# Optimization experiments

Measured on AMD Instinct MI355X. Metric: run time of the kernel, lower is better.

Reference implementation:

```python
import jax, jax.numpy as jnp
import numpy as np

N = 50000   # nodes
E = 500000  # edges
D = 128     # enc_dim == Hout
INIT_W = 0.1


def _lin_w(k, din, dout):
    return jax.random.normal(k, (dout, din), jnp.float32) * INIT_W


def setup_inputs() -> dict:
    key = jax.random.key(0)
    ks = jax.random.split(key, 16)
    inp = {
        "x": jax.random.normal(ks[0], (N, D), jnp.float32),
        "src": jax.random.randint(ks[1], (E,), 0, N),
        "dst": jax.random.randint(ks[2], (E,), 0, N),
        # encoders (Linear enc_dim -> enc_dim)
        "WencK": _lin_w(ks[3], D, D), "bencK": jnp.zeros((D,), jnp.float32),
        "WencP1": _lin_w(ks[4], D, D), "bencP1": jnp.zeros((D,), jnp.float32),
        "WencP2": _lin_w(ks[5], D, D), "bencP2": jnp.zeros((D,), jnp.float32),
        # Kfun: Linear-Tanh-Linear-ReLU-Linear
        "K0W": _lin_w(ks[6], D, D), "K0b": jnp.zeros((D,), jnp.float32),
        "K1W": _lin_w(ks[7], D, D), "K1b": jnp.zeros((D,), jnp.float32),
        "K2W": _lin_w(ks[8], D, D), "K2b": jnp.zeros((D,), jnp.float32),
        # Ufun: Linear-Tanh-Linear-ReLU-Linear
        "U0W": _lin_w(ks[9], D, D), "U0b": jnp.zeros((D,), jnp.float32),
        "U1W": _lin_w(ks[10], D, D), "U1b": jnp.zeros((D,), jnp.float32),
        "U2W": _lin_w(ks[11], D, D), "U2b": jnp.zeros((D,), jnp.float32),
    }
    return inp


def _mlp3(h, W0, b0, W1, b1, W2, b2):
    h = jnp.tanh(h @ W0.T + b0)
    h = jax.nn.relu(h @ W1.T + b1)
    return h @ W2.T + b2


def reference(x, src, dst,
              WencK, bencK, WencP1, bencP1, WencP2, bencP2,
              K0W, K0b, K1W, K1b, K2W, K2b,
              U0W, U0b, U1W, U1b, U2W, U2b):
    # getK: encode nodes, copy_u + sum to dst, node MLP
    h1 = x @ WencK.T + bencK                                   # [N, D]
    h1_agg = jax.ops.segment_sum(h1[src], dst, num_segments=N)  # [N, D]
    Knode = _mlp3(h1_agg, K0W, K0b, K1W, K1b, K2W, K2b)         # [N, D]
    # getU: u_add_v on encoded features, edge MLP
    p1 = x @ WencP1.T + bencP1
    p2 = x @ WencP2.T + bencP2
    Eedge = _mlp3(p1[src] + p2[dst], U0W, U0b, U1W, U1b, U2W, U2b)  # [E, D]
    # getH: u_mul_e + sum to dst
    Enew = jax.ops.segment_sum(Knode[src] * Eedge, dst, num_segments=N)  # [N, D]
    return jnp.sum(Enew)
```

## Files before the change

### kernel.cpp

```cpp
#include <hip/hip_runtime.h>
#include <math.h>

#define NN 50000
#define NE 500000
#define DD 128
#define STR 136
#define NSCAN (2 * NN)
#define NBLK ((NSCAN + 1023) / 1024)

typedef __attribute__((ext_vector_type(8))) short short8;
typedef __attribute__((ext_vector_type(4))) float floatx4;

__device__ __forceinline__ float bf2f(unsigned short u) {
    unsigned v = ((unsigned)u) << 16;
    float f;
    __builtin_memcpy(&f, &v, 4);
    return f;
}
__device__ __forceinline__ unsigned short f2bf(float f) {
    unsigned x;
    __builtin_memcpy(&x, &f, 4);
    x += 0x7FFF + ((x >> 16) & 1);
    return (unsigned short)(x >> 16);
}
__device__ __forceinline__ float fast_tanh(float x) {
    float t = __builtin_amdgcn_exp2f(x * 2.88539008177793f);
    return 1.f - 2.f * __builtin_amdgcn_rcpf(t + 1.f);
}

__global__ __launch_bounds__(256) void composite_kernel(
    const float* __restrict__ U0W, const float* __restrict__ WencP1,
    const float* __restrict__ WencP2, const float* __restrict__ K0W,
    const float* __restrict__ WencK,
    const float* __restrict__ bp1, const float* __restrict__ bp2,
    const float* __restrict__ U0b, const float* __restrict__ bk,
    const float* __restrict__ U2b,
    float* __restrict__ comp, float* __restrict__ bvecs)
{
    int b = blockIdx.x;
    int t = threadIdx.x;
    if (b == 6) {
        if (t < 128) {
            float s1 = 0.f, s2 = 0.f;
            for (int k = 0; k < DD; ++k) {
                s1 += U0W[t * DD + k] * (bp1[k] + bp2[k]);
                s2 += K0W[t * DD + k] * bk[k];
            }
            bvecs[t] = s1 + U0b[t];
            bvecs[128 + t] = s2;
            int f = (t & 64) + 16 * (t & 3) + ((t & 63) >> 2);
            bvecs[256 + t] = U2b[f];
        }
        return;
    }
    __shared__ float Bs[DD * DD];
    int mat = b >> 1, half = b & 1;
    const float* A = (mat == 2) ? K0W : U0W;
    const float* B = (mat == 0) ? WencP1 : (mat == 1) ? WencP2 : WencK;
    float* C = comp + (size_t)mat * DD * DD;
    for (int i = 0; i < 64; ++i)
        Bs[i * 256 + t] = B[i * 256 + t];
    __syncthreads();
    int row = half * 64 + (t >> 2);
    int j0 = (t & 3) * 32;
    float acc[32];
    #pragma unroll
    for (int jj = 0; jj < 32; ++jj) acc[jj] = 0.f;
    for (int k = 0; k < DD; ++k) {
        float a = A[row * DD + k];
        #pragma unroll
        for (int jj = 0; jj < 32; ++jj)
            acc[jj] += a * Bs[k * DD + j0 + jj];
    }
    #pragma unroll
    for (int jj = 0; jj < 32; ++jj) C[row * DD + j0 + jj] = acc[jj];
}

__global__ __launch_bounds__(256) void preconv_kernel(
    const float* __restrict__ comp, const float* __restrict__ K1W,
    const float* __restrict__ K2W, const float* __restrict__ U2W,
    const float* __restrict__ U1W, unsigned short* __restrict__ out)
{
    int g = blockIdx.x * 256 + threadIdx.x;
    if (g >= 7 * 2048) return;
    int m = g >> 11;
    int rem = g & 2047;
    int kt = rem >> 9, nt = (rem >> 6) & 7, lane = rem & 63;
    const float* W;
    bool perm = false, tr = false;
    switch (m) {
        case 0: W = comp; break;
        case 1: W = comp + 16384; break;
        case 2: W = comp + 32768; break;
        case 3: W = K1W; perm = true; break;
        case 4: W = K2W; perm = true; break;
        case 5: W = U2W; perm = true; tr = true; break;
        default: W = U1W; break;
    }
    int n = nt * 16 + (lane & 15);
    #pragma unroll
    for (int j = 0; j < 8; ++j) {
        int ks = kt * 32 + (lane >> 4) * 8 + j;
        int f = perm ? (ks & 64) + 16 * (ks & 3) + ((ks & 63) >> 2) : ks;
        float v = tr ? W[f * DD + n] : W[n * DD + f];
        out[(size_t)g * 8 + j] = f2bf(v);
    }
}

__global__ __launch_bounds__(256) void hist_kernel(
    const int* __restrict__ src, const int* __restrict__ dst,
    int* __restrict__ cnt_dst, int* __restrict__ cnt_src,
    int* __restrict__ rank_d, int* __restrict__ rank_s)
{
    int e = blockIdx.x * 256 + threadIdx.x;
    if (e < NE) {
        rank_d[e] = atomicAdd(&cnt_dst[dst[e]], 1);
        rank_s[e] = atomicAdd(&cnt_src[src[e]], 1);
    }
}

__global__ __launch_bounds__(1024) void scan1_kernel(
    const int* __restrict__ cnt, int* __restrict__ base, int* __restrict__ bsum)
{
    __shared__ int wsum[16];
    int t = threadIdx.x;
    int i = blockIdx.x * 1024 + t;
    int v = (i < NSCAN) ? cnt[i] : 0;
    int lane = t & 63, w = t >> 6;
    int x = v;
    #pragma unroll
    for (int off = 1; off < 64; off <<= 1) {
        int y = __shfl_up(x, off);
        if (lane >= off) x += y;
    }
    if (lane == 63) wsum[w] = x;
    __syncthreads();
    if (w == 0) {
        int s = (lane < 16) ? wsum[lane] : 0;
        #pragma unroll
        for (int off = 1; off < 16; off <<= 1) {
            int y = __shfl_up(s, off);
            if (lane >= off) s += y;
        }
        if (lane < 16) wsum[lane] = s;
    }
    __syncthreads();
    int wavebase = (w == 0) ? 0 : wsum[w - 1];
    int incl = wavebase + x;
    if (i < NSCAN) base[i] = incl - v;
    if (t == 1023) bsum[blockIdx.x] = incl;
}

__global__ __launch_bounds__(128) void scan2_kernel(
    int* __restrict__ bsum, float* __restrict__ out)
{
    if (threadIdx.x == 0 && blockIdx.x == 0) *out = 0.f;
    __shared__ int wsum[2];
    int t = threadIdx.x;
    int v = (t < NBLK) ? bsum[t] : 0;
    int lane = t & 63, w = t >> 6;
    int x = v;
    #pragma unroll
    for (int off = 1; off < 64; off <<= 1) {
        int y = __shfl_up(x, off);
        if (lane >= off) x += y;
    }
    if (lane == 63) wsum[w] = x;
    __syncthreads();
    int wavebase = (w == 0) ? 0 : wsum[0];
    int incl = wavebase + x;
    if (t < NBLK) bsum[t] = incl - v;
}

__global__ __launch_bounds__(1024) void scan3_kernel(
    int* __restrict__ base, const int* __restrict__ bsum)
{
    int i = blockIdx.x * 1024 + threadIdx.x;
    if (i < NSCAN) base[i] += bsum[blockIdx.x];
}

__global__ __launch_bounds__(256) void place_kernel(
    const int* __restrict__ src, const int* __restrict__ dst,
    const int* __restrict__ base,
    const int* __restrict__ rank_d, const int* __restrict__ rank_s,
    int* __restrict__ sorted_src_bydst,
    int* __restrict__ sorted_dst_bysrc, int* __restrict__ sorted_sid_bysrc)
{
    int e = blockIdx.x * 256 + threadIdx.x;
    if (e < NE) {
        int s = src[e], d = dst[e];
        sorted_src_bydst[base[d] + rank_d[e]] = s;
        int p = base[NN + s] + rank_s[e] - NE;
        sorted_dst_bysrc[p] = d;
        sorted_sid_bysrc[p] = s;
    }
}

__global__ __launch_bounds__(256) void enc_kernel(
    const float* __restrict__ x, const unsigned short* __restrict__ wf,
    const float* __restrict__ bvecs,
    unsigned short* __restrict__ q1, unsigned short* __restrict__ q2,
    unsigned short* __restrict__ xbf)
{
    __shared__ unsigned short A[128 * STR];
    const int t = threadIdx.x;
    const int lane = t & 63, w = t >> 6;
    const int wm = w >> 1, wn = w & 1;
    const int c = lane & 15, q = lane >> 4;
    const int row0 = blockIdx.x * 128;

    #pragma unroll
    for (int i = 0; i < 16; ++i) {
        int idx = i * 256 + t;
        int r = idx >> 5, ch = idx & 31;
        int gr = row0 + r;
        ushort4 v4 = {0, 0, 0, 0};
        if (gr < NN) {
            float4 f = *(const float4*)&x[(size_t)gr * DD + ch * 4];
            v4.x = f2bf(f.x); v4.y = f2bf(f.y); v4.z = f2bf(f.z); v4.w = f2bf(f.w);
            *(ushort4*)&xbf[(size_t)gr * DD + ch * 4] = v4;
        }
        *(ushort4*)&A[r * STR + ch * 4] = v4;
    }
    __syncthreads();

    for (int l = 0; l < 2; ++l) {
        floatx4 acc[4][4];
        #pragma unroll
        for (int i = 0; i < 4; ++i)
            #pragma unroll
            for (int j = 0; j < 4; ++j)
                acc[i][j] = (floatx4){0.f, 0.f, 0.f, 0.f};
        const short8* W8 = (const short8*)(wf + (size_t)l * 16384);
        #pragma unroll
        for (int kt = 0; kt < 4; ++kt) {
            short8 af[4], bfr[4];
            #pragma unroll
            for (int i = 0; i < 4; ++i)
                af[i] = *(const short8*)&A[(wm * 64 + i * 16 + c) * STR + kt * 32 + q * 8];
            #pragma unroll
            for (int j = 0; j < 4; ++j)
                bfr[j] = W8[(kt * 8 + wn * 4 + j) * 64 + lane];
            #pragma unroll
            for (int i = 0; i < 4; ++i)
                #pragma unroll
                for (int j = 0; j < 4; ++j)
                    acc[i][j] = __builtin_amdgcn_mfma_f32_16x16x32_bf16(af[i], bfr[j], acc[i][j], 0, 0, 0);
        }
        unsigned short* pp = (l == 0) ? q1 : q2;
        float bv[4];
        #pragma unroll
        for (int j = 0; j < 4; ++j)
            bv[j] = (l == 0) ? bvecs[c + 16 * j + 64 * wn] : 0.f;

        #pragma unroll
        for (int i = 0; i < 4; ++i)
            #pragma unroll
            for (int r = 0; r < 4; ++r) {
                int node = row0 + wm * 64 + i * 16 + 4 * q + r;
                if (node < NN) {
                    #pragma unroll
                    for (int j = 0; j < 4; ++j)
                        pp[(size_t)node * DD + c + 16 * j + 64 * wn] = f2bf(acc[i][j][r] + bv[j]);
                }
            }
    }
}

__global__ __launch_bounds__(256) void agg_kernel(
    const unsigned short* __restrict__ xbf,
    const int* __restrict__ base, const int* __restrict__ cnt,
    const int* __restrict__ sorted_src,
    unsigned short* __restrict__ xagg)
{
    int wave = blockIdx.x * 4 + (threadIdx.x >> 6);
    int lane = threadIdx.x & 63;
    if (wave >= NN) return;
    int lo = base[wave];
    int hi = lo + cnt[wave];
    float ax = 0.f, ay = 0.f;
    for (int off = lo; off < hi; off += 64) {
        int myid = (off + lane < hi) ? sorted_src[off + lane] : 0;
        int nk = min(64, hi - off);
        int k = 0;
        for (; k + 4 <= nk; k += 4) {
            int s0 = __shfl(myid, k);
            int s1 = __shfl(myid, k + 1);
            int s2 = __shfl(myid, k + 2);
            int s3 = __shfl(myid, k + 3);
            ushort2 v0 = *(const ushort2*)&xbf[(size_t)s0 * DD + lane * 2];
            ushort2 v1 = *(const ushort2*)&xbf[(size_t)s1 * DD + lane * 2];
            ushort2 v2 = *(const ushort2*)&xbf[(size_t)s2 * DD + lane * 2];
            ushort2 v3 = *(const ushort2*)&xbf[(size_t)s3 * DD + lane * 2];
            ax += bf2f(v0.x) + bf2f(v1.x) + bf2f(v2.x) + bf2f(v3.x);
            ay += bf2f(v0.y) + bf2f(v1.y) + bf2f(v2.y) + bf2f(v3.y);
        }
        for (; k < nk; ++k) {
            int s = __shfl(myid, k);
            ushort2 v = *(const ushort2*)&xbf[(size_t)s * DD + lane * 2];
            ax += bf2f(v.x);
            ay += bf2f(v.y);
        }
    }
    ushort2 o;
    o.x = f2bf(ax); o.y = f2bf(ay);
    *(ushort2*)&xagg[(size_t)wave * DD + lane * 2] = o;
}

__global__ __launch_bounds__(256) void node_kernel(
    const unsigned short* __restrict__ xagg, const unsigned short* __restrict__ wf,
    const int* __restrict__ cnt, const float* __restrict__ bvecs,
    const float* __restrict__ K0b, const float* __restrict__ K1b,
    const float* __restrict__ K2b,
    unsigned short* __restrict__ Km, float* __restrict__ kb)
{
    __shared__ unsigned short A[128 * STR];
    const int t = threadIdx.x;
    const int lane = t & 63, w = t >> 6;
    const int wm = w >> 1, wn = w & 1;
    const int c = lane & 15, q = lane >> 4;
    const int row0 = blockIdx.x * 128;

    #pragma unroll
    for (int i = 0; i < 8; ++i) {
        int idx = i * 256 + t;
        int r = idx >> 4, ch = idx & 15;
        int gr = row0 + r;
        short8 v = (short8){0,0,0,0,0,0,0,0};
        if (gr < NN) v = *(const short8*)&xagg[(size_t)gr * DD + ch * 8];
        *(short8*)&A[r * STR + ch * 8] = v;
    }
    __syncthreads();

    for (int l = 0; l < 4; ++l) {
        floatx4 acc[4][4];
        #pragma unroll
        for (int i = 0; i < 4; ++i)
            #pragma unroll
            for (int j = 0; j < 4; ++j)
                acc[i][j] = (floatx4){0.f, 0.f, 0.f, 0.f};
        const short8* W8 = (const short8*)(wf + (size_t)(2 + l) * 16384);
        #pragma unroll
        for (int kt = 0; kt < 4; ++kt) {
            short8 af[4], bfr[4];
            #pragma unroll
            for (int i = 0; i < 4; ++i)
                af[i] = *(const short8*)&A[(wm * 64 + i * 16 + c) * STR + kt * 32 + q * 8];
            #pragma unroll
            for (int j = 0; j < 4; ++j)
                bfr[j] = W8[(kt * 8 + wn * 4 + j) * 64 + lane];
            #pragma unroll
            for (int i = 0; i < 4; ++i)
                #pragma unroll
                for (int j = 0; j < 4; ++j)
                    acc[i][j] = __builtin_amdgcn_mfma_f32_16x16x32_bf16(af[i], bfr[j], acc[i][j], 0, 0, 0);
        }

        if (l < 3) {
            const float* bb = (l == 0) ? K0b : (l == 1) ? K1b : K2b;
            float bv[4];
            #pragma unroll
            for (int j = 0; j < 4; ++j) bv[j] = bb[c + 16 * j + 64 * wn];
            float bvv[4];
            #pragma unroll
            for (int j = 0; j < 4; ++j)
                bvv[j] = (l == 0) ? bvecs[128 + c + 16 * j + 64 * wn] : 0.f;

            __syncthreads();
            #pragma unroll
            for (int i = 0; i < 4; ++i)
                #pragma unroll
                for (int r = 0; r < 4; ++r) {
                    int node = row0 + wm * 64 + i * 16 + 4 * q + r;
                    float cn = (l == 0) ? (float)((node < NN) ? cnt[node] : 0) : 0.f;
                    float v0 = acc[i][0][r] + bv[0] + cn * bvv[0];
                    float v1 = acc[i][1][r] + bv[1] + cn * bvv[1];
                    float v2 = acc[i][2][r] + bv[2] + cn * bvv[2];
                    float v3 = acc[i][3][r] + bv[3] + cn * bvv[3];
                    if (l == 0) {
                        v0 = fast_tanh(v0); v1 = fast_tanh(v1);
                        v2 = fast_tanh(v2); v3 = fast_tanh(v3);
                    } else if (l == 1) {
                        v0 = fmaxf(v0, 0.f); v1 = fmaxf(v1, 0.f);
                        v2 = fmaxf(v2, 0.f); v3 = fmaxf(v3, 0.f);
                    }
                    ushort4 pk;
                    pk.x = f2bf(v0); pk.y = f2bf(v1); pk.z = f2bf(v2); pk.w = f2bf(v3);
                    int m = wm * 64 + i * 16 + 4 * q + r;
                    *(ushort4*)&A[m * STR + 4 * c + 64 * wn] = pk;
                }
            __syncthreads();

            if (l == 2) {
                if (t < 128) {
                    int node = row0 + t;
                    if (node < NN) {
                        float s = 0.f;
                        #pragma unroll
                        for (int ch = 0; ch < 16; ++ch) {
                            short8 v = *(const short8*)&A[t * STR + ch * 8];
                            #pragma unroll
                            for (int e = 0; e < 8; ++e)
                                s += bf2f((unsigned short)v[e]) * bvecs[256 + ch * 8 + e];
                        }
                        kb[node] = s;
                    }
                }
            }
        } else {
            #pragma unroll
            for (int i = 0; i < 4; ++i)
                #pragma unroll
                for (int r = 0; r < 4; ++r) {
                    int node = row0 + wm * 64 + i * 16 + 4 * q + r;
                    if (node < NN) {
                        ushort4 pk;
                        pk.x = f2bf(acc[i][0][r]);
                        pk.y = f2bf(acc[i][1][r]);
                        pk.z = f2bf(acc[i][2][r]);
                        pk.w = f2bf(acc[i][3][r]);
                        *(ushort4*)&Km[(size_t)node * DD + 4 * c + 64 * wn] = pk;
                    }
                }
        }
    }
}

__global__ __launch_bounds__(256) void edge_kernel(
    const unsigned short* __restrict__ q1, const unsigned short* __restrict__ q2,
    const unsigned short* __restrict__ Km, const float* __restrict__ kb,
    const int* __restrict__ sorted_sid, const int* __restrict__ sorted_dst,
    const unsigned short* __restrict__ wf, const float* __restrict__ U1b,
    float* __restrict__ out)
{
    __shared__ unsigned short A[128 * STR];
    __shared__ int sidx[128];
    __shared__ int didx[128];
    __shared__ float red[4];
    const int t = threadIdx.x;
    const int lane = t & 63, w = t >> 6;
    const int wm = w >> 1, wn = w & 1;
    const int c = lane & 15, q = lane >> 4;
    const int e0 = blockIdx.x * 128;

    if (t < 128) {
        int e = e0 + t;
        sidx[t] = (e < NE) ? sorted_sid[e] : -1;
        didx[t] = (e < NE) ? sorted_dst[e] : 0;
    }
    __syncthreads();

    float part = 0.f;
    if (t < 128 && sidx[t] >= 0) part += kb[sidx[t]];

    #pragma unroll
    for (int i = 0; i < 8; ++i) {
        int idx = i * 256 + t;
        int r = idx >> 4, ch = idx & 15;
        int s = sidx[r];
        short8 o8 = (short8){0,0,0,0,0,0,0,0};
        if (s >= 0) {
            short8 a8 = *(const short8*)&q1[(size_t)s * DD + ch * 8];
            short8 b8 = *(const short8*)&q2[(size_t)didx[r] * DD + ch * 8];
            #pragma unroll
            for (int k = 0; k < 8; ++k)
                o8[k] = (short)f2bf(fast_tanh(bf2f((unsigned short)a8[k]) + bf2f((unsigned short)b8[k])));
        }
        *(short8*)&A[r * STR + ch * 8] = o8;
    }
    __syncthreads();

    floatx4 acc[4][4];
    #pragma unroll
    for (int i = 0; i < 4; ++i)
        #pragma unroll
        for (int j = 0; j < 4; ++j)
            acc[i][j] = (floatx4){0.f, 0.f, 0.f, 0.f};
    const short8* W8 = (const short8*)(wf + (size_t)6 * 16384);
    #pragma unroll
    for (int kt = 0; kt < 4; ++kt) {
        short8 af[4], bfr[4];
        #pragma unroll
        for (int i = 0; i < 4; ++i)
            af[i] = *(const short8*)&A[(wm * 64 + i * 16 + c) * STR + kt * 32 + q * 8];
        #pragma unroll
        for (int j = 0; j < 4; ++j)
            bfr[j] = W8[(kt * 8 + wn * 4 + j) * 64 + lane];
        #pragma unroll
        for (int i = 0; i < 4; ++i)
            #pragma unroll
            for (int j = 0; j < 4; ++j)
                acc[i][j] = __builtin_amdgcn_mfma_f32_16x16x32_bf16(af[i], bfr[j], acc[i][j], 0, 0, 0);
    }
    float bv[4];
    #pragma unroll
    for (int j = 0; j < 4; ++j) bv[j] = U1b[c + 16 * j + 64 * wn];

    #pragma unroll
    for (int i = 0; i < 4; ++i)
        #pragma unroll
        for (int r = 0; r < 4; ++r) {
            int m = wm * 64 + i * 16 + 4 * q + r;
            int s = sidx[m];
            if (s >= 0) {
                ushort4 km4 = *(const ushort4*)&Km[(size_t)s * DD + 4 * c + 64 * wn];
                part += fmaxf(acc[i][0][r] + bv[0], 0.f) * bf2f(km4.x)
                      + fmaxf(acc[i][1][r] + bv[1], 0.f) * bf2f(km4.y)
                      + fmaxf(acc[i][2][r] + bv[2], 0.f) * bf2f(km4.z)
                      + fmaxf(acc[i][3][r] + bv[3], 0.f) * bf2f(km4.w);
            }
        }

    #pragma unroll
    for (int off = 32; off > 0; off >>= 1)
        part += __shfl_down(part, off);
    if (lane == 0) red[w] = part;
    __syncthreads();
    if (t == 0)
        atomicAdd(out, red[0] + red[1] + red[2] + red[3]);
}

extern "C" void kernel_launch(void* const* d_in, const int* in_sizes, int n_in,
                              void* d_out, int out_size, void* d_ws, size_t ws_size,
                              hipStream_t stream)
{
    const float* x     = (const float*)d_in[0];
    const int*   src   = (const int*)  d_in[1];
    const int*   dst   = (const int*)  d_in[2];
    const float* WencK = (const float*)d_in[3];
    const float* bencK = (const float*)d_in[4];
    const float* WencP1= (const float*)d_in[5];
    const float* bencP1= (const float*)d_in[6];
    const float* WencP2= (const float*)d_in[7];
    const float* bencP2= (const float*)d_in[8];
    const float* K0W   = (const float*)d_in[9];
    const float* K0b   = (const float*)d_in[10];
    const float* K1W   = (const float*)d_in[11];
    const float* K1b   = (const float*)d_in[12];
    const float* K2W   = (const float*)d_in[13];
    const float* K2b   = (const float*)d_in[14];
    const float* U0W   = (const float*)d_in[15];
    const float* U0b   = (const float*)d_in[16];
    const float* U1W   = (const float*)d_in[17];
    const float* U1b   = (const float*)d_in[18];
    const float* U2W   = (const float*)d_in[19];
    const float* U2b   = (const float*)d_in[20];

    char* ws = (char*)d_ws;
    unsigned short* wfrag = (unsigned short*)ws;
    float* comp  = (float*)(ws + 0x40000);
    float* bvecs = (float*)(ws + 0x70000);
    unsigned short* xbf  = (unsigned short*)(ws + 0x71000);
    unsigned short* q1   = xbf + (size_t)NN * DD;
    unsigned short* q2   = q1 + (size_t)NN * DD;
    unsigned short* Kmg  = q2 + (size_t)NN * DD;
    unsigned short* xagg = Kmg + (size_t)NN * DD;
    float* kb       = (float*)(xagg + (size_t)NN * DD);
    int* cnt_dst    = (int*)(kb + NN);
    int* cnt_src    = cnt_dst + NN;
    int* base       = cnt_src + NN;
    int* bsum       = base + NSCAN;
    int* rank_d     = bsum + 128;
    int* rank_s     = rank_d + NE;
    int* sorted_src_bydst = rank_s + NE;
    int* sorted_dst_bysrc = sorted_src_bydst + NE;
    int* sorted_sid_bysrc = sorted_dst_bysrc + NE;

    hipMemsetAsync(cnt_dst, 0, 2 * NN * sizeof(int), stream);

    composite_kernel<<<7, 256, 0, stream>>>(
        U0W, WencP1, WencP2, K0W, WencK, bencP1, bencP2, U0b, bencK, U2b,
        comp, bvecs);

    preconv_kernel<<<(7 * 2048 + 255) / 256, 256, 0, stream>>>(
        comp, K1W, K2W, U2W, U1W, wfrag);

    hist_kernel<<<(NE + 255) / 256, 256, 0, stream>>>(
        src, dst, cnt_dst, cnt_src, rank_d, rank_s);

    scan1_kernel<<<NBLK, 1024, 0, stream>>>(cnt_dst, base, bsum);
    scan2_kernel<<<1, 128, 0, stream>>>(bsum, (float*)d_out);
    scan3_kernel<<<NBLK, 1024, 0, stream>>>(base, bsum);

    place_kernel<<<(NE + 255) / 256, 256, 0, stream>>>(
        src, dst, base, rank_d, rank_s,
        sorted_src_bydst, sorted_dst_bysrc, sorted_sid_bysrc);

    enc_kernel<<<(NN + 127) / 128, 256, 0, stream>>>(
        x, wfrag, bvecs, q1, q2, xbf);

    agg_kernel<<<(NN + 3) / 4, 256, 0, stream>>>(
        xbf, base, cnt_dst, sorted_src_bydst, xagg);

    node_kernel<<<(NN + 127) / 128, 256, 0, stream>>>(
        xagg, wfrag, cnt_dst, bvecs, K0b, K1b, K2b, Kmg, kb);

    edge_kernel<<<(NE + 127) / 128, 256, 0, stream>>>(
        q1, q2, Kmg, kb, sorted_sid_bysrc, sorted_dst_bysrc, wfrag, U1b,
        (float*)d_out);
}
```

Before: 342.2 us.

## Merge independent setup kernels into fewer launches and pack edge index pairs

Merges several small, independent kernels into shared launches that pick their role by block index. Histogram, x-to-bf16 conversion and weight composition share one launch. Preconversion shares a launch with the first scan pass, and the encoder GEMM shares one with the node MLP. Edge (src,dst) pairs are stored as a single int2 array, and each edge block now processes two 128-edge tiles, which halves the number of atomics on the output. The goal is to cut launch count and serial gaps. The cost is less parallelism per launch and a larger shared-memory footprint in merged blocks, since the 64KB Bs array is now declared in histogram blocks too, which may reduce occupancy.

```diff
diff --git a/kernel.cpp b/kernel.cpp
--- a/kernel.cpp
+++ b/kernel.cpp
@@ -1,4 +1,5 @@
 #include <hip/hip_runtime.h>
+#include <hip/hip_bf16.h>
 #include <math.h>
 
 #define NN 50000
@@ -6,7 +7,11 @@
 #define DD 128
 #define STR 136
 #define NSCAN (2 * NN)
-#define NBLK ((NSCAN + 1023) / 1024)
+#define SCAN_BLK ((NSCAN + 1023) / 1024)
+#define HIST_BLK ((NE + 255) / 256)
+#define CVT_BLK  ((NN * DD + 4095) / 4096)
+#define PRECONV_BLK ((7 * 2048 + 1023) / 1024)
+#define ENC_BLK  ((NN + 127) / 128)
 
 typedef __attribute__((ext_vector_type(8))) short short8;
 typedef __attribute__((ext_vector_type(4))) float floatx4;
@@ -28,7 +33,11 @@
     return 1.f - 2.f * __builtin_amdgcn_rcpf(t + 1.f);
 }
 
-__global__ __launch_bounds__(256) void composite_kernel(
+__global__ __launch_bounds__(256) void k1_kernel(
+    const int* __restrict__ src, const int* __restrict__ dst,
+    int* __restrict__ cnt_dst, int* __restrict__ cnt_src,
+    int* __restrict__ rank_d, int* __restrict__ rank_s,
+    const float* __restrict__ x, unsigned short* __restrict__ xbf,
     const float* __restrict__ U0W, const float* __restrict__ WencP1,
     const float* __restrict__ WencP2, const float* __restrict__ K0W,
     const float* __restrict__ WencK,
@@ -37,8 +46,35 @@
     const float* __restrict__ U2b,
     float* __restrict__ comp, float* __restrict__ bvecs)
 {
-    int b = blockIdx.x;
+    __shared__ float Bs[DD * DD];
+    int blk = blockIdx.x;
     int t = threadIdx.x;
+
+    if (blk < HIST_BLK) {
+        int e = blk * 256 + t;
+        if (e < NE) {
+            rank_d[e] = atomicAdd(&cnt_dst[dst[e]], 1);
+            rank_s[e] = atomicAdd(&cnt_src[src[e]], 1);
+        }
+        return;
+    }
+    if (blk < HIST_BLK + CVT_BLK) {
+        int base = (blk - HIST_BLK) * 4096;
+        #pragma unroll
+        for (int j = 0; j < 4; ++j) {
+            int idx = base + (j * 256 + t) * 4;
+            if (idx < NN * DD) {
+                float4 f = *(const float4*)&x[idx];
+                ushort4 v4;
+                v4.x = f2bf(f.x); v4.y = f2bf(f.y);
+                v4.z = f2bf(f.z); v4.w = f2bf(f.w);
+                *(ushort4*)&xbf[idx] = v4;
+            }
+        }
+        return;
+    }
+
+    int b = blk - (HIST_BLK + CVT_BLK);
     if (b == 6) {
         if (t < 128) {
             float s1 = 0.f, s2 = 0.f;
@@ -53,7 +89,6 @@
         }
         return;
     }
-    __shared__ float Bs[DD * DD];
     int mat = b >> 1, half = b & 1;
     const float* A = (mat == 2) ? K0W : U0W;
     const float* B = (mat == 0) ? WencP1 : (mat == 1) ? WencP2 : WencK;
@@ -76,56 +111,76 @@
     for (int jj = 0; jj < 32; ++jj) C[row * DD + j0 + jj] = acc[jj];
 }
 
-__global__ __launch_bounds__(256) void preconv_kernel(
+__global__ __launch_bounds__(1024) void k2_kernel(
     const float* __restrict__ comp, const float* __restrict__ K1W,
     const float* __restrict__ K2W, const float* __restrict__ U2W,
-    const float* __restrict__ U1W, unsigned short* __restrict__ out)
-{
-    int g = blockIdx.x * 256 + threadIdx.x;
-    if (g >= 7 * 2048) return;
-    int m = g >> 11;
-    int rem = g & 2047;
-    int kt = rem >> 9, nt = (rem >> 6) & 7, lane = rem & 63;
-    const float* W;
-    bool perm = false, tr = false;
-    switch (m) {
-        case 0: W = comp; break;
-        case 1: W = comp + 16384; break;
-        case 2: W = comp + 32768; break;
-        case 3: W = K1W; perm = true; break;
-        case 4: W = K2W; perm = true; break;
-        case 5: W = U2W; perm = true; tr = true; break;
-        default: W = U1W; break;
-    }
-    int n = nt * 16 + (lane & 15);
+    const float* __restrict__ U1W, unsigned short* __restrict__ wfrag,
+    const int* __restrict__ cnt, int* __restrict__ base, int* __restrict__ bsum)
+{
+    int t = threadIdx.x;
+    if (blockIdx.x < PRECONV_BLK) {
+        int g = blockIdx.x * 1024 + t;
+        if (g >= 7 * 2048) return;
+        int m = g >> 11;
+        int rem = g & 2047;
+        int kt = rem >> 9, nt = (rem >> 6) & 7, lane = rem & 63;
+        const float* W;
+        bool perm = false, tr = false;
+        switch (m) {
+            case 0: W = comp; break;
+            case 1: W = comp + 16384; break;
+            case 2: W = comp + 32768; break;
+            case 3: W = K1W; perm = true; break;
+            case 4: W = K2W; perm = true; break;
+            case 5: W = U2W; perm = true; tr = true; break;
+            default: W = U1W; break;
+        }
+        int n = nt * 16 + (lane & 15);
+        #pragma unroll
+        for (int j = 0; j < 8; ++j) {
+            int ks = kt * 32 + (lane >> 4) * 8 + j;
+            int f = perm ? (ks & 64) + 16 * (ks & 3) + ((ks & 63) >> 2) : ks;
+            float v = tr ? W[f * DD + n] : W[n * DD + f];
+            wfrag[(size_t)g * 8 + j] = f2bf(v);
+        }
+        return;
+    }
+    __shared__ int wsum[16];
+    int sb = blockIdx.x - PRECONV_BLK;
+    int i = sb * 1024 + t;
+    int v = (i < NSCAN) ? cnt[i] : 0;
+    int lane = t & 63, w = t >> 6;
+    int xv = v;
     #pragma unroll
-    for (int j = 0; j < 8; ++j) {
-        int ks = kt * 32 + (lane >> 4) * 8 + j;
-        int f = perm ? (ks & 64) + 16 * (ks & 3) + ((ks & 63) >> 2) : ks;
-        float v = tr ? W[f * DD + n] : W[n * DD + f];
-        out[(size_t)g * 8 + j] = f2bf(v);
-    }
-}
-
-__global__ __launch_bounds__(256) void hist_kernel(
-    const int* __restrict__ src, const int* __restrict__ dst,
-    int* __restrict__ cnt_dst, int* __restrict__ cnt_src,
-    int* __restrict__ rank_d, int* __restrict__ rank_s)
-{
-    int e = blockIdx.x * 256 + threadIdx.x;
-    if (e < NE) {
-        rank_d[e] = atomicAdd(&cnt_dst[dst[e]], 1);
-        rank_s[e] = atomicAdd(&cnt_src[src[e]], 1);
-    }
-}
-
-__global__ __launch_bounds__(1024) void scan1_kernel(
-    const int* __restrict__ cnt, int* __restrict__ base, int* __restrict__ bsum)
-{
-    __shared__ int wsum[16];
+    for (int off = 1; off < 64; off <<= 1) {
+        int y = __shfl_up(xv, off);
+        if (lane >= off) xv += y;
+    }
+    if (lane == 63) wsum[w] = xv;
+    __syncthreads();
+    if (w == 0) {
+        int s = (lane < 16) ? wsum[lane] : 0;
+        #pragma unroll
+        for (int off = 1; off < 16; off <<= 1) {
+            int y = __shfl_up(s, off);
+            if (lane >= off) s += y;
+        }
+        if (lane < 16) wsum[lane] = s;
+    }
+    __syncthreads();
+    int wavebase = (w == 0) ? 0 : wsum[w - 1];
+    int incl = wavebase + xv;
+    if (i < NSCAN) base[i] = incl - v;
+    if (t == 1023) bsum[sb] = incl;
+}
+
+__global__ __launch_bounds__(128) void scan2_kernel(
+    int* __restrict__ bsum, float* __restrict__ out)
+{
+    if (threadIdx.x == 0 && blockIdx.x == 0) *out = 0.f;
+    __shared__ int wsum[2];
     int t = threadIdx.x;
-    int i = blockIdx.x * 1024 + t;
-    int v = (i < NSCAN) ? cnt[i] : 0;
+    int v = (t < SCAN_BLK) ? bsum[t] : 0;
     int lane = t & 63, w = t >> 6;
     int x = v;
     #pragma unroll
@@ -135,41 +190,9 @@
     }
     if (lane == 63) wsum[w] = x;
     __syncthreads();
-    if (w == 0) {
-        int s = (lane < 16) ? wsum[lane] : 0;
-        #pragma unroll
-        for (int off = 1; off < 16; off <<= 1) {
-            int y = __shfl_up(s, off);
-            if (lane >= off) s += y;
-        }
-        if (lane < 16) wsum[lane] = s;
-    }
-    __syncthreads();
-    int wavebase = (w == 0) ? 0 : wsum[w - 1];
-    int incl = wavebase + x;
-    if (i < NSCAN) base[i] = incl - v;
-    if (t == 1023) bsum[blockIdx.x] = incl;
-}
-
-__global__ __launch_bounds__(128) void scan2_kernel(
-    int* __restrict__ bsum, float* __restrict__ out)
-{
-    if (threadIdx.x == 0 && blockIdx.x == 0) *out = 0.f;
-    __shared__ int wsum[2];
-    int t = threadIdx.x;
-    int v = (t < NBLK) ? bsum[t] : 0;
-    int lane = t & 63, w = t >> 6;
-    int x = v;
-    #pragma unroll
-    for (int off = 1; off < 64; off <<= 1) {
-        int y = __shfl_up(x, off);
-        if (lane >= off) x += y;
-    }
-    if (lane == 63) wsum[w] = x;
-    __syncthreads();
     int wavebase = (w == 0) ? 0 : wsum[0];
     int incl = wavebase + x;
-    if (t < NBLK) bsum[t] = incl - v;
+    if (t < SCAN_BLK) bsum[t] = incl - v;
 }
 
 __global__ __launch_bounds__(1024) void scan3_kernel(
@@ -183,87 +206,14 @@
     const int* __restrict__ src, const int* __restrict__ dst,
     const int* __restrict__ base,
     const int* __restrict__ rank_d, const int* __restrict__ rank_s,
-    int* __restrict__ sorted_src_bydst,
-    int* __restrict__ sorted_dst_bysrc, int* __restrict__ sorted_sid_bysrc)
+    int* __restrict__ sorted_src_bydst, int2* __restrict__ epairs)
 {
     int e = blockIdx.x * 256 + threadIdx.x;
     if (e < NE) {
         int s = src[e], d = dst[e];
         sorted_src_bydst[base[d] + rank_d[e]] = s;
         int p = base[NN + s] + rank_s[e] - NE;
-        sorted_dst_bysrc[p] = d;
-        sorted_sid_bysrc[p] = s;
-    }
-}
-
-__global__ __launch_bounds__(256) void enc_kernel(
-    const float* __restrict__ x, const unsigned short* __restrict__ wf,
-    const float* __restrict__ bvecs,
-    unsigned short* __restrict__ q1, unsigned short* __restrict__ q2,
-    unsigned short* __restrict__ xbf)
-{
-    __shared__ unsigned short A[128 * STR];
-    const int t = threadIdx.x;
-    const int lane = t & 63, w = t >> 6;
-    const int wm = w >> 1, wn = w & 1;
-    const int c = lane & 15, q = lane >> 4;
-    const int row0 = blockIdx.x * 128;
-
-    #pragma unroll
-    for (int i = 0; i < 16; ++i) {
-        int idx = i * 256 + t;
-        int r = idx >> 5, ch = idx & 31;
-        int gr = row0 + r;
-        ushort4 v4 = {0, 0, 0, 0};
-        if (gr < NN) {
-            float4 f = *(const float4*)&x[(size_t)gr * DD + ch * 4];
-            v4.x = f2bf(f.x); v4.y = f2bf(f.y); v4.z = f2bf(f.z); v4.w = f2bf(f.w);
-            *(ushort4*)&xbf[(size_t)gr * DD + ch * 4] = v4;
-        }
-        *(ushort4*)&A[r * STR + ch * 4] = v4;
-    }
-    __syncthreads();
-
-    for (int l = 0; l < 2; ++l) {
-        floatx4 acc[4][4];
-        #pragma unroll
-        for (int i = 0; i < 4; ++i)
-            #pragma unroll
-            for (int j = 0; j < 4; ++j)
-                acc[i][j] = (floatx4){0.f, 0.f, 0.f, 0.f};
-        const short8* W8 = (const short8*)(wf + (size_t)l * 16384);
-        #pragma unroll
-        for (int kt = 0; kt < 4; ++kt) {
-            short8 af[4], bfr[4];
-            #pragma unroll
-            for (int i = 0; i < 4; ++i)
-                af[i] = *(const short8*)&A[(wm * 64 + i * 16 + c) * STR + kt * 32 + q * 8];
-            #pragma unroll
-            for (int j = 0; j < 4; ++j)
-                bfr[j] = W8[(kt * 8 + wn * 4 + j) * 64 + lane];
-            #pragma unroll
-            for (int i = 0; i < 4; ++i)
-                #pragma unroll
-                for (int j = 0; j < 4; ++j)
-                    acc[i][j] = __builtin_amdgcn_mfma_f32_16x16x32_bf16(af[i], bfr[j], acc[i][j], 0, 0, 0);
-        }
-        unsigned short* pp = (l == 0) ? q1 : q2;
-        float bv[4];
-        #pragma unroll
-        for (int j = 0; j < 4; ++j)
-            bv[j] = (l == 0) ? bvecs[c + 16 * j + 64 * wn] : 0.f;
-
-        #pragma unroll
-        for (int i = 0; i < 4; ++i)
-            #pragma unroll
-            for (int r = 0; r < 4; ++r) {
-                int node = row0 + wm * 64 + i * 16 + 4 * q + r;
-                if (node < NN) {
-                    #pragma unroll
-                    for (int j = 0; j < 4; ++j)
-                        pp[(size_t)node * DD + c + 16 * j + 64 * wn] = f2bf(acc[i][j][r] + bv[j]);
-                }
-            }
+        epairs[p] = make_int2(s, d);
     }
 }
 
@@ -307,11 +257,13 @@
     *(ushort2*)&xagg[(size_t)wave * DD + lane * 2] = o;
 }
 
-__global__ __launch_bounds__(256) void node_kernel(
-    const unsigned short* __restrict__ xagg, const unsigned short* __restrict__ wf,
-    const int* __restrict__ cnt, const float* __restrict__ bvecs,
+__global__ __launch_bounds__(256) void encnode_kernel(
+    const float* __restrict__ x, const unsigned short* __restrict__ xagg,
+    const unsigned short* __restrict__ wf, const float* __restrict__ bvecs,
+    const int* __restrict__ cnt,
     const float* __restrict__ K0b, const float* __restrict__ K1b,
     const float* __restrict__ K2b,
+    unsigned short* __restrict__ q1, unsigned short* __restrict__ q2,
     unsigned short* __restrict__ Km, float* __restrict__ kb)
 {
     __shared__ unsigned short A[128 * STR];
@@ -319,8 +271,69 @@
     const int lane = t & 63, w = t >> 6;
     const int wm = w >> 1, wn = w & 1;
     const int c = lane & 15, q = lane >> 4;
-    const int row0 = blockIdx.x * 128;
-
+
+    if (blockIdx.x < ENC_BLK) {
+        const int row0 = blockIdx.x * 128;
+        #pragma unroll
+        for (int i = 0; i < 16; ++i) {
+            int idx = i * 256 + t;
+            int r = idx >> 5, ch = idx & 31;
+            int gr = row0 + r;
+            ushort4 v4 = {0, 0, 0, 0};
+            if (gr < NN) {
+                float4 f = *(const float4*)&x[(size_t)gr * DD + ch * 4];
+                v4.x = f2bf(f.x); v4.y = f2bf(f.y);
+                v4.z = f2bf(f.z); v4.w = f2bf(f.w);
+            }
+            *(ushort4*)&A[r * STR + ch * 4] = v4;
+        }
+        __syncthreads();
+
+        for (int l = 0; l < 2; ++l) {
+            floatx4 acc[4][4];
+            #pragma unroll
+            for (int i = 0; i < 4; ++i)
+                #pragma unroll
+                for (int j = 0; j < 4; ++j)
+                    acc[i][j] = (floatx4){0.f, 0.f, 0.f, 0.f};
+            const short8* W8 = (const short8*)(wf + (size_t)l * 16384);
+            #pragma unroll
+            for (int kt = 0; kt < 4; ++kt) {
+                short8 af[4], bfr[4];
+                #pragma unroll
+                for (int i = 0; i < 4; ++i)
+                    af[i] = *(const short8*)&A[(wm * 64 + i * 16 + c) * STR + kt * 32 + q * 8];
+                #pragma unroll
+                for (int j = 0; j < 4; ++j)
+                    bfr[j] = W8[(kt * 8 + wn * 4 + j) * 64 + lane];
+                #pragma unroll
+                for (int i = 0; i < 4; ++i)
+                    #pragma unroll
+                    for (int j = 0; j < 4; ++j)
+                        acc[i][j] = __builtin_amdgcn_mfma_f32_16x16x32_bf16(af[i], bfr[j], acc[i][j], 0, 0, 0);
+            }
+            unsigned short* pp = (l == 0) ? q1 : q2;
+            float bv[4];
+            #pragma unroll
+            for (int j = 0; j < 4; ++j)
+                bv[j] = (l == 0) ? bvecs[c + 16 * j + 64 * wn] : 0.f;
+
+            #pragma unroll
+            for (int i = 0; i < 4; ++i)
+                #pragma unroll
+                for (int r = 0; r < 4; ++r) {
+                    int node = row0 + wm * 64 + i * 16 + 4 * q + r;
+                    if (node < NN) {
+                        #pragma unroll
+                        for (int j = 0; j < 4; ++j)
+                            pp[(size_t)node * DD + c + 16 * j + 64 * wn] = f2bf(acc[i][j][r] + bv[j]);
+                    }
+                }
+        }
+        return;
+    }
+
+    const int row0 = (blockIdx.x - ENC_BLK) * 128;
     #pragma unroll
     for (int i = 0; i < 8; ++i) {
         int idx = i * 256 + t;
@@ -429,7 +442,7 @@
 __global__ __launch_bounds__(256) void edge_kernel(
     const unsigned short* __restrict__ q1, const unsigned short* __restrict__ q2,
     const unsigned short* __restrict__ Km, const float* __restrict__ kb,
-    const int* __restrict__ sorted_sid, const int* __restrict__ sorted_dst,
+    const int2* __restrict__ epairs,
     const unsigned short* __restrict__ wf, const float* __restrict__ U1b,
     float* __restrict__ out)
 {
@@ -441,75 +454,91 @@
     const int lane = t & 63, w = t >> 6;
     const int wm = w >> 1, wn = w & 1;
     const int c = lane & 15, q = lane >> 4;
-    const int e0 = blockIdx.x * 128;
-
-    if (t < 128) {
-        int e = e0 + t;
-        sidx[t] = (e < NE) ? sorted_sid[e] : -1;
-        didx[t] = (e < NE) ? sorted_dst[e] : 0;
-    }
-    __syncthreads();
-
-    float part = 0.f;
-    if (t < 128 && sidx[t] >= 0) part += kb[sidx[t]];
-
-    #pragma unroll
-    for (int i = 0; i < 8; ++i) {
-        int idx = i * 256 + t;
-        int r = idx >> 4, ch = idx & 15;
-        int s = sidx[r];
-        short8 o8 = (short8){0,0,0,0,0,0,0,0};
-        if (s >= 0) {
-            short8 a8 = *(const short8*)&q1[(size_t)s * DD + ch * 8];
-            short8 b8 = *(const short8*)&q2[(size_t)didx[r] * DD + ch * 8];
-            #pragma unroll
-            for (int k = 0; k < 8; ++k)
-                o8[k] = (short)f2bf(fast_tanh(bf2f((unsigned short)a8[k]) + bf2f((unsigned short)b8[k])));
-        }
-        *(short8*)&A[r * STR + ch * 8] = o8;
-    }
-    __syncthreads();
-
-    floatx4 acc[4][4];
-    #pragma unroll
-    for (int i = 0; i < 4; ++i)
-        #pragma unroll
-        for (int j = 0; j < 4; ++j)
-            acc[i][j] = (floatx4){0.f, 0.f, 0.f, 0.f};
-    const short8* W8 = (const short8*)(wf + (size_t)6 * 16384);
-    #pragma unroll
-    for (int kt = 0; kt < 4; ++kt) {
-        short8 af[4], bfr[4];
-        #pragma unroll
-        for (int i = 0; i < 4; ++i)
-            af[i] = *(const short8*)&A[(wm * 64 + i * 16 + c) * STR + kt * 32 + q * 8];
-        #pragma unroll
-        for (int j = 0; j < 4; ++j)
-            bfr[j] = W8[(kt * 8 + wn * 4 + j) * 64 + lane];
-        #pragma unroll
-        for (int i = 0; i < 4; ++i)
-            #pragma unroll
-            for (int j = 0; j < 4; ++j)
-                acc[i][j] = __builtin_amdgcn_mfma_f32_16x16x32_bf16(af[i], bfr[j], acc[i][j], 0, 0, 0);
-    }
+
     float bv[4];
     #pragma unroll
     for (int j = 0; j < 4; ++j) bv[j] = U1b[c + 16 * j + 64 * wn];
 
-    #pragma unroll
-    for (int i = 0; i < 4; ++i)
-        #pragma unroll
-        for (int r = 0; r < 4; ++r) {
-            int m = wm * 64 + i * 16 + 4 * q + r;
-            int s = sidx[m];
+    float part = 0.f;
+
+    for (int tile = 0; tile < 2; ++tile) {
+        const int e0 = blockIdx.x * 256 + tile * 128;
+        if (tile) __syncthreads();
+        if (t < 128) {
+            int e = e0 + t;
+            if (e < NE) {
+                int2 p = epairs[e];
+                sidx[t] = p.x;
+                didx[t] = p.y;
+            } else {
+                sidx[t] = -1;
+                didx[t] = 0;
+            }
+        }
+        __syncthreads();
+
+        if (t < 128 && sidx[t] >= 0) part += kb[sidx[t]];
+
+        #pragma unroll
+        for (int i = 0; i < 8; ++i) {
+            int idx = i * 256 + t;
+            int r = idx >> 4, ch = idx & 15;
+            int s = sidx[r];
+            int o32[4] = {0, 0, 0, 0};
             if (s >= 0) {
-                ushort4 km4 = *(const ushort4*)&Km[(size_t)s * DD + 4 * c + 64 * wn];
-                part += fmaxf(acc[i][0][r] + bv[0], 0.f) * bf2f(km4.x)
-                      + fmaxf(acc[i][1][r] + bv[1], 0.f) * bf2f(km4.y)
-                      + fmaxf(acc[i][2][r] + bv[2], 0.f) * bf2f(km4.z)
-                      + fmaxf(acc[i][3][r] + bv[3], 0.f) * bf2f(km4.w);
-            }
-        }
+                short8 a8 = *(const short8*)&q1[(size_t)s * DD + ch * 8];
+                short8 b8 = *(const short8*)&q2[(size_t)didx[r] * DD + ch * 8];
+                #pragma unroll
+                for (int k = 0; k < 8; k += 2) {
+                    float2 u;
+                    u.x = fast_tanh(bf2f((unsigned short)a8[k])     + bf2f((unsigned short)b8[k]));
+                    u.y = fast_tanh(bf2f((unsigned short)a8[k + 1]) + bf2f((unsigned short)b8[k + 1]));
+                    __hip_bfloat162 hb = __float22bfloat162_rn(u);
+                    __builtin_memcpy(&o32[k >> 1], &hb, 4);
+                }
+            }
+            *(int4*)&A[r * STR + ch * 8] = *(int4*)o32;
+        }
+        __syncthreads();
+
+        floatx4 acc[4][4];
+        #pragma unroll
+        for (int i = 0; i < 4; ++i)
+            #pragma unroll
+            for (int j = 0; j < 4; ++j)
+                acc[i][j] = (floatx4){0.f, 0.f, 0.f, 0.f};
+        const short8* W8 = (const short8*)(wf + (size_t)6 * 16384);
+        #pragma unroll
+        for (int kt = 0; kt < 4; ++kt) {
+            short8 af[4], bfr[4];
+            #pragma unroll
+            for (int i = 0; i < 4; ++i)
+                af[i] = *(const short8*)&A[(wm * 64 + i * 16 + c) * STR + kt * 32 + q * 8];
+            #pragma unroll
+            for (int j = 0; j < 4; ++j)
+                bfr[j] = W8[(kt * 8 + wn * 4 + j) * 64 + lane];
+            #pragma unroll
+            for (int i = 0; i < 4; ++i)
+                #pragma unroll
+                for (int j = 0; j < 4; ++j)
+                    acc[i][j] = __builtin_amdgcn_mfma_f32_16x16x32_bf16(af[i], bfr[j], acc[i][j], 0, 0, 0);
+        }
+
+        #pragma unroll
+        for (int i = 0; i < 4; ++i)
+            #pragma unroll
+            for (int r = 0; r < 4; ++r) {
+                int m = wm * 64 + i * 16 + 4 * q + r;
+                int s = sidx[m];
+                if (s >= 0) {
+                    ushort4 km4 = *(const ushort4*)&Km[(size_t)s * DD + 4 * c + 64 * wn];
+                    part += fmaxf(acc[i][0][r] + bv[0], 0.f) * bf2f(km4.x)
+                          + fmaxf(acc[i][1][r] + bv[1], 0.f) * bf2f(km4.y)
+                          + fmaxf(acc[i][2][r] + bv[2], 0.f) * bf2f(km4.z)
+                          + fmaxf(acc[i][3][r] + bv[3], 0.f) * bf2f(km4.w);
+                }
+            }
+    }
 
     #pragma unroll
     for (int off = 32; off > 0; off >>= 1)
@@ -563,39 +592,30 @@
     int* rank_d     = bsum + 128;
     int* rank_s     = rank_d + NE;
     int* sorted_src_bydst = rank_s + NE;
-    int* sorted_dst_bysrc = sorted_src_bydst + NE;
-    int* sorted_sid_bysrc = sorted_dst_bysrc + NE;
+    int2* epairs    = (int2*)(sorted_src_bydst + NE);
 
     hipMemsetAsync(cnt_dst, 0, 2 * NN * sizeof(int), stream);
 
-    composite_kernel<<<7, 256, 0, stream>>>(
+    k1_kernel<<<HIST_BLK + CVT_BLK + 7, 256, 0, stream>>>(
+        src, dst, cnt_dst, cnt_src, rank_d, rank_s, x, xbf,
         U0W, WencP1, WencP2, K0W, WencK, bencP1, bencP2, U0b, bencK, U2b,
         comp, bvecs);
 
-    preconv_kernel<<<(7 * 2048 + 255) / 256, 256, 0, stream>>>(
-        comp, K1W, K2W, U2W, U1W, wfrag);
-
-    hist_kernel<<<(NE + 255) / 256, 256, 0, stream>>>(
-        src, dst, cnt_dst, cnt_src, rank_d, rank_s);
-
-    scan1_kernel<<<NBLK, 1024, 0, stream>>>(cnt_dst, base, bsum);
+    k2_kernel<<<PRECONV_BLK + SCAN_BLK, 1024, 0, stream>>>(
+        comp, K1W, K2W, U2W, U1W, wfrag, cnt_dst, base, bsum);
+
     scan2_kernel<<<1, 128, 0, stream>>>(bsum, (float*)d_out);
-    scan3_kernel<<<NBLK, 1024, 0, stream>>>(base, bsum);
-
-    place_kernel<<<(NE + 255) / 256, 256, 0, stream>>>(
-        src, dst, base, rank_d, rank_s,
-        sorted_src_bydst, sorted_dst_bysrc, sorted_sid_bysrc);
-
-    enc_kernel<<<(NN + 127) / 128, 256, 0, stream>>>(
-        x, wfrag, bvecs, q1, q2, xbf);
+    scan3_kernel<<<SCAN_BLK, 1024, 0, stream>>>(base, bsum);
+
+    place_kernel<<<HIST_BLK, 256, 0, stream>>>(
+        src, dst, base, rank_d, rank_s, sorted_src_bydst, epairs);
 
     agg_kernel<<<(NN + 3) / 4, 256, 0, stream>>>(
         xbf, base, cnt_dst, sorted_src_bydst, xagg);
 
-    node_kernel<<<(NN + 127) / 128, 256, 0, stream>>>(
-        xagg, wfrag, cnt_dst, bvecs, K0b, K1b, K2b, Kmg, kb);
-
-    edge_kernel<<<(NE + 127) / 128, 256, 0, stream>>>(
-        q1, q2, Kmg, kb, sorted_sid_bysrc, sorted_dst_bysrc, wfrag, U1b,
-        (float*)d_out);
-}
+    encnode_kernel<<<2 * ENC_BLK, 256, 0, stream>>>(
+        x, xagg, wfrag, bvecs, cnt_dst, K0b, K1b, K2b, q1, q2, Kmg, kb);
+
+    edge_kernel<<<(NE + 255) / 256, 256, 0, stream>>>(
+        q1, q2, Kmg, kb, epairs, wfrag, U1b, (float*)d_out);
+}
```

After: 340.7 us. Within noise of the previous version (-0.4%).
